# Optimization experiments

Measured on AMD Instinct MI355X. Metric: run time of the kernel, lower is better.

The kernel has to match this reference:

```python
import jax, jax.numpy as jnp
import numpy as np

HEADS = 8


def setup_inputs() -> dict:
    key = jax.random.key(0)
    k1, k2, k3, k4, k5, k6 = jax.random.split(key, 6)
    B, S, E = 2, 2048, 512
    D = E // HEADS
    return {
        "values": jax.random.normal(k1, (B, S, E), dtype=jnp.float32),
        "keys": jax.random.normal(k2, (B, S, E), dtype=jnp.float32),
        "queries": jax.random.normal(k3, (B, S, E), dtype=jnp.float32),
        "mask": jax.random.randint(k4, (B, 1, 1, S), 0, 2, dtype=jnp.int32),
        "W_v": jax.random.normal(k5, (D, D), dtype=jnp.float32) * (1.0 / np.sqrt(D)),
        "W_o": jax.random.normal(k6, (E, E), dtype=jnp.float32) * (1.0 / np.sqrt(E)),
        "b_o": jnp.zeros((E,), dtype=jnp.float32),
    }


def reference(values, keys, queries, mask, W_v, W_o, b_o):
    B, S, E = queries.shape
    H = HEADS
    D = E // H
    # reshape to (b, s, h, d) and apply the SAME W_v linear to v, k, q
    # (faithful to the original, which calls self.values on all three)
    v = jnp.einsum('bshd,ed->bshe', values.reshape(B, -1, H, D), W_v)
    k = jnp.einsum('bshd,ed->bshe', keys.reshape(B, -1, H, D), W_v)
    q = jnp.einsum('bshd,ed->bshe', queries.reshape(B, -1, H, D), W_v)
    # unscaled attention scores (original has no 1/sqrt(d))
    energy = jnp.einsum('bqhd,bkhd->bhqk', q, k)  # (b, h, q, k)
    energy = jnp.where(mask == 0, -jnp.inf, energy)
    attn = jax.nn.softmax(energy, axis=3)
    out = jnp.einsum('bhqk,bkhd->bqhd', attn, v)  # (b, q, h, d)
    out = out.reshape(B, S, E)
    return out @ W_o.T + b_o
```

## Files before the change

kernel.cpp:

```cpp
#include <hip/hip_runtime.h>


#define B_ 2
#define S_ 2048
#define E_ 512
#define H_ 8
#define D_ 64

typedef unsigned short ushort_t;
typedef __attribute__((ext_vector_type(8))) short short8;
typedef __attribute__((ext_vector_type(8))) _Float16 half8;
typedef __attribute__((ext_vector_type(4))) float f32x4;

__device__ __forceinline__ ushort_t f2bs(float x) {
    union { float f; unsigned int u; } a; a.f = x;
    unsigned int u = a.u;
    u += 0x7fffu + ((u >> 16) & 1u);
    return (ushort_t)(u >> 16);
}
__device__ __forceinline__ float bs2f(ushort_t h) {
    union { unsigned int u; float f; } a; a.u = ((unsigned int)h) << 16;
    return a.f;
}
__device__ __forceinline__ ushort_t f2hs(float x) {
    _Float16 h = (_Float16)x;
    ushort_t u; __builtin_memcpy(&u, &h, 2);
    return u;
}
__device__ __forceinline__ void split16(const float4* g, ushort_t* hi, ushort_t* lo) {
    #pragma unroll
    for (int q = 0; q < 4; ++q) {
        float4 f = g[q];
        float vv[4] = {f.x, f.y, f.z, f.w};
        #pragma unroll
        for (int j = 0; j < 4; ++j) {
            ushort_t h = f2bs(vv[j]);
            hi[q * 4 + j] = h;
            lo[q * 4 + j] = f2bs(vv[j] - bs2f(h));
        }
    }
}

__global__ void __launch_bounds__(256) proj_mfma(
    const float* __restrict__ quer, const float* __restrict__ keys,
    const float* __restrict__ vals, const float* __restrict__ Wv,
    ushort_t* __restrict__ qf, ushort_t* __restrict__ kf,
    ushort_t* __restrict__ vt)
{
    __shared__ ushort_t Ah[64 * 72], Al[64 * 72];
    __shared__ ushort_t Bh[64 * 72], Bl[64 * 72];
    const int tens = blockIdx.y;
    const float* src = tens == 0 ? quer : (tens == 1 ? keys : vals);
    const int bx = blockIdx.x;
    const int st = bx & 31, bh = bx >> 5;
    const int b = bh >> 3, h = bh & 7;
    const int s0 = st * 64;
    const int t = threadIdx.x;

    {
        int e = t >> 2, dg = (t & 3) * 16;
        ushort_t th[16], tl[16];
        split16((const float4*)(Wv + e * 64 + dg), th, tl);
        *(uint4*)&Bh[e * 72 + dg] = *(uint4*)th;  *(uint4*)&Bh[e * 72 + dg + 8] = *(uint4*)(th + 8);
        *(uint4*)&Bl[e * 72 + dg] = *(uint4*)tl;  *(uint4*)&Bl[e * 72 + dg + 8] = *(uint4*)(tl + 8);
    }
    {
        int row = t >> 2, cg = (t & 3) * 16;
        const float* g = src + ((size_t)b * S_ + s0 + row) * 512 + h * 64 + cg;
        ushort_t th[16], tl[16];
        split16((const float4*)g, th, tl);
        *(uint4*)&Ah[row * 72 + cg] = *(uint4*)th;  *(uint4*)&Ah[row * 72 + cg + 8] = *(uint4*)(th + 8);
        *(uint4*)&Al[row * 72 + cg] = *(uint4*)tl;  *(uint4*)&Al[row * 72 + cg + 8] = *(uint4*)(tl + 8);
    }
    __syncthreads();

    const int w = t >> 6, lm = t & 15, quad = (t >> 4) & 3;
    f32x4 acc[4];
    #pragma unroll
    for (int nt = 0; nt < 4; ++nt) acc[nt] = (f32x4){0.f, 0.f, 0.f, 0.f};

    #pragma unroll
    for (int kk = 0; kk < 2; ++kk) {
        short8 ah = *(const short8*)&Ah[(w * 16 + lm) * 72 + kk * 32 + quad * 8];
        short8 al = *(const short8*)&Al[(w * 16 + lm) * 72 + kk * 32 + quad * 8];
        #pragma unroll
        for (int nt = 0; nt < 4; ++nt) {
            short8 bh8 = *(const short8*)&Bh[(nt * 16 + lm) * 72 + kk * 32 + quad * 8];
            short8 bl8 = *(const short8*)&Bl[(nt * 16 + lm) * 72 + kk * 32 + quad * 8];
            acc[nt] = __builtin_amdgcn_mfma_f32_16x16x32_bf16(ah, bh8, acc[nt], 0, 0, 0);
            acc[nt] = __builtin_amdgcn_mfma_f32_16x16x32_bf16(al, bh8, acc[nt], 0, 0, 0);
            acc[nt] = __builtin_amdgcn_mfma_f32_16x16x32_bf16(ah, bl8, acc[nt], 0, 0, 0);
        }
    }

    if (tens < 2) {
        ushort_t* dst = tens == 0 ? qf : kf;
        #pragma unroll
        for (int nt = 0; nt < 4; ++nt) {
            #pragma unroll
            for (int r = 0; r < 4; ++r) {
                size_t addr = ((size_t)bh * S_ + s0 + w * 16 + quad * 4 + r) * 64 + nt * 16 + lm;
                dst[addr] = f2hs(acc[nt][r]);
            }
        }
    } else {
        #pragma unroll
        for (int nt = 0; nt < 4; ++nt) {
            unsigned int p0 = (unsigned int)f2bs(acc[nt][0]) | ((unsigned int)f2bs(acc[nt][1]) << 16);
            unsigned int p1 = (unsigned int)f2bs(acc[nt][2]) | ((unsigned int)f2bs(acc[nt][3]) << 16);
            uint2 pk; pk.x = p0; pk.y = p1;
            size_t addr = ((size_t)bh * 64 + nt * 16 + lm) * S_ + s0 + w * 16 + quad * 4;
            *(uint2*)&vt[addr] = pk;
        }
    }
}

__global__ void __launch_bounds__(256) attn_mfma(
    const ushort_t* __restrict__ qf, const ushort_t* __restrict__ kf,
    const ushort_t* __restrict__ vt, const int* __restrict__ mask,
    ushort_t* __restrict__ ctx)
{
    __shared__ ushort_t Ks[64 * 72];
    __shared__ ushort_t Vt[64 * 72];
    __shared__ ushort_t Ps[4 * 16 * 72];
    __shared__ float    mbias[64];

    const int bx = blockIdx.x;
    const int qt = bx & 31;
    const int bh = bx >> 5;
    const int b  = bh >> 3, h = bh & 7;
    const int t  = threadIdx.x;
    const int w = t >> 6, lm = t & 15, quad = (t >> 4) & 3;
    const int q0 = qt * 64;
    const int wbase = w * 16 * 72;

    half8 aq[2];
    {
        size_t qrow = ((size_t)bh * S_ + q0 + w * 16 + lm) * 64 + quad * 8;
        #pragma unroll
        for (int kk = 0; kk < 2; ++kk)
            aq[kk] = *(const half8*)&qf[qrow + kk * 32];
    }
    short8 ones;
    #pragma unroll
    for (int j = 0; j < 8; ++j) ones[j] = (short)0x3F80;

    f32x4 acc[4];
    #pragma unroll
    for (int nt = 0; nt < 4; ++nt) acc[nt] = (f32x4){0.f, 0.f, 0.f, 0.f};
    f32x4 acc_l = (f32x4){0.f, 0.f, 0.f, 0.f};

    for (int kc = 0; kc < S_ / 64; ++kc) {
        __syncthreads();
        {
            int row = t >> 2, cg = (t & 3) * 16;
            size_t gaddr = ((size_t)bh * S_ + kc * 64 + row) * 64 + cg;
            *(uint4*)&Ks[row * 72 + cg]     = *(const uint4*)&kf[gaddr];
            *(uint4*)&Ks[row * 72 + cg + 8] = *(const uint4*)&kf[gaddr + 8];
        }
        {
            int row = t >> 2, cg = (t & 3) * 16;
            size_t gaddr = ((size_t)bh * 64 + row) * S_ + kc * 64 + cg;
            *(uint4*)&Vt[row * 72 + cg]     = *(const uint4*)&vt[gaddr];
            *(uint4*)&Vt[row * 72 + cg + 8] = *(const uint4*)&vt[gaddr + 8];
        }
        if (t < 64) mbias[t] = mask[b * S_ + kc * 64 + t] ? -64.f : -1e30f;
        __syncthreads();

        #pragma unroll
        for (int nt = 0; nt < 4; ++nt) {
            f32x4 s = (f32x4){0.f, 0.f, 0.f, 0.f};
            #pragma unroll
            for (int kk = 0; kk < 2; ++kk) {
                half8 bk = *(const half8*)&Ks[(nt * 16 + lm) * 72 + kk * 32 + quad * 8];
                s = __builtin_amdgcn_mfma_f32_16x16x32_f16(aq[kk], bk, s, 0, 0, 0);
            }
            float mv = mbias[nt * 16 + lm];
            #pragma unroll
            for (int r = 0; r < 4; ++r) {
                float p = __expf(s[r] + mv);
                Ps[wbase + (quad * 4 + r) * 72 + nt * 16 + lm] = f2bs(p);
            }
        }
        __builtin_amdgcn_s_waitcnt(0);

        #pragma unroll
        for (int kk = 0; kk < 2; ++kk) {
            short8 ap = *(const short8*)&Ps[wbase + lm * 72 + kk * 32 + quad * 8];
            #pragma unroll
            for (int nt = 0; nt < 4; ++nt) {
                short8 bv = *(const short8*)&Vt[(nt * 16 + lm) * 72 + kk * 32 + quad * 8];
                acc[nt] = __builtin_amdgcn_mfma_f32_16x16x32_bf16(ap, bv, acc[nt], 0, 0, 0);
            }
            acc_l = __builtin_amdgcn_mfma_f32_16x16x32_bf16(ap, ones, acc_l, 0, 0, 0);
        }
    }

    #pragma unroll
    for (int r = 0; r < 4; ++r) {
        float inv = 1.f / acc_l[r];
        int s = q0 + w * 16 + quad * 4 + r;
        #pragma unroll
        for (int nt = 0; nt < 4; ++nt) {
            int d = nt * 16 + lm;
            ctx[((size_t)b * S_ + s) * E_ + h * D_ + d] = f2bs(acc[nt][r] * inv);
        }
    }
}

__global__ void __launch_bounds__(256) outproj_mfma(
    const ushort_t* __restrict__ ctx, const float* __restrict__ Wo,
    const float* __restrict__ bo, float* __restrict__ out)
{
    __shared__ ushort_t As[64 * 72];
    __shared__ ushort_t Bs[64 * 72];
    const int m0 = blockIdx.x * 64, n0 = blockIdx.y * 64;
    const int t = threadIdx.x;
    const int w = t >> 6, lm = t & 15, quad = (t >> 4) & 3;

    f32x4 acc[4];
    #pragma unroll
    for (int nt = 0; nt < 4; ++nt) acc[nt] = (f32x4){0.f, 0.f, 0.f, 0.f};

    for (int kc = 0; kc < E_ / 64; ++kc) {
        __syncthreads();
        {
            int row = t >> 2, cg = (t & 3) * 16;
            const ushort_t* g = ctx + (size_t)(m0 + row) * E_ + kc * 64 + cg;
            *(uint4*)&As[row * 72 + cg]     = *(const uint4*)g;
            *(uint4*)&As[row * 72 + cg + 8] = *(const uint4*)(g + 8);
        }
        {
            int n = t >> 2, kg = (t & 3) * 16;
            const float4* g = (const float4*)(Wo + (size_t)(n0 + n) * E_ + kc * 64 + kg);
            ushort_t tmp[16];
            #pragma unroll
            for (int q = 0; q < 4; ++q) {
                float4 f = g[q];
                tmp[q * 4 + 0] = f2bs(f.x); tmp[q * 4 + 1] = f2bs(f.y);
                tmp[q * 4 + 2] = f2bs(f.z); tmp[q * 4 + 3] = f2bs(f.w);
            }
            *(uint4*)&Bs[n * 72 + kg]     = *(uint4*)tmp;
            *(uint4*)&Bs[n * 72 + kg + 8] = *(uint4*)(tmp + 8);
        }
        __syncthreads();

        #pragma unroll
        for (int kk = 0; kk < 2; ++kk) {
            short8 a = *(const short8*)&As[(w * 16 + lm) * 72 + kk * 32 + quad * 8];
            #pragma unroll
            for (int nt = 0; nt < 4; ++nt) {
                short8 bb = *(const short8*)&Bs[(nt * 16 + lm) * 72 + kk * 32 + quad * 8];
                acc[nt] = __builtin_amdgcn_mfma_f32_16x16x32_bf16(a, bb, acc[nt], 0, 0, 0);
            }
        }
    }

    #pragma unroll
    for (int nt = 0; nt < 4; ++nt) {
        float bias = bo[n0 + nt * 16 + lm];
        #pragma unroll
        for (int r = 0; r < 4; ++r) {
            int m = m0 + w * 16 + quad * 4 + r;
            out[(size_t)m * E_ + n0 + nt * 16 + lm] = acc[nt][r] + bias;
        }
    }
}

extern "C" void kernel_launch(void* const* d_in, const int* in_sizes, int n_in,
                              void* d_out, int out_size, void* d_ws, size_t ws_size,
                              hipStream_t stream) {
    const float* vals = (const float*)d_in[0];
    const float* keys = (const float*)d_in[1];
    const float* quer = (const float*)d_in[2];
    const int*   mask = (const int*)d_in[3];
    const float* Wv   = (const float*)d_in[4];
    const float* Wo   = (const float*)d_in[5];
    const float* bo   = (const float*)d_in[6];
    float* out = (float*)d_out;

    const size_t N = (size_t)B_ * H_ * S_ * D_;
    ushort_t* ws  = (ushort_t*)d_ws;
    ushort_t* qf  = ws;
    ushort_t* kf  = ws + N;
    ushort_t* vt  = ws + 2 * N;
    ushort_t* ctx = ws + 3 * N;

    proj_mfma<<<dim3(B_ * H_ * (S_ / 64), 3), 256, 0, stream>>>(
        quer, keys, vals, Wv, qf, kf, vt);
    attn_mfma<<<B_ * H_ * (S_ / 64), 256, 0, stream>>>(qf, kf, vt, mask, ctx);
    outproj_mfma<<<dim3((B_ * S_) / 64, E_ / 64), 256, 0, stream>>>(ctx, Wo, bo, out);
}
```

Baseline: 147.8 us.

## Double-buffer K/V tiles in attention with register prefetch and transposed score MFMA

Attention K/V and mask tiles are now double-buffered in shared memory. The next tile is loaded into registers while the current tile is computed, then written to the alternate buffer, which cuts the loop to one barrier per iteration and hides global load latency. The score MFMA operands are also swapped, so each lane holds four consecutive keys and can read the mask bias as a vector and store P with one packed 8-byte write instead of four scalar stores. The cost is twice the LDS for K/V, more live registers, and a narrower waitcnt (lgkmcnt only).

```diff
diff --git a/kernel.cpp b/kernel.cpp
--- a/kernel.cpp
+++ b/kernel.cpp
@@ -120,26 +120,29 @@
     const ushort_t* __restrict__ vt, const int* __restrict__ mask,
     ushort_t* __restrict__ ctx)
 {
-    __shared__ ushort_t Ks[64 * 72];
-    __shared__ ushort_t Vt[64 * 72];
+    __shared__ ushort_t Ks[2][64 * 72];
+    __shared__ ushort_t Vt[2][64 * 72];
     __shared__ ushort_t Ps[4 * 16 * 72];
-    __shared__ float    mbias[64];
+    __shared__ float    mb[2][64];
 
     const int bx = blockIdx.x;
     const int qt = bx & 31;
     const int bh = bx >> 5;
-    const int b  = bh >> 3, h = bh & 7;
+    const int b  = bh >> 3;
     const int t  = threadIdx.x;
     const int w = t >> 6, lm = t & 15, quad = (t >> 4) & 3;
     const int q0 = qt * 64;
     const int wbase = w * 16 * 72;
 
+    const int srow = t >> 2, scg = (t & 3) * 16;
+    const size_t kgbase = ((size_t)bh * S_ + srow) * 64 + scg;
+    const size_t vgbase = ((size_t)bh * 64 + srow) * S_ + scg;
+
     half8 aq[2];
     {
         size_t qrow = ((size_t)bh * S_ + q0 + w * 16 + lm) * 64 + quad * 8;
-        #pragma unroll
-        for (int kk = 0; kk < 2; ++kk)
-            aq[kk] = *(const half8*)&qf[qrow + kk * 32];
+        aq[0] = *(const half8*)&qf[qrow];
+        aq[1] = *(const half8*)&qf[qrow + 32];
     }
     short8 ones;
     #pragma unroll
@@ -150,52 +153,77 @@
     for (int nt = 0; nt < 4; ++nt) acc[nt] = (f32x4){0.f, 0.f, 0.f, 0.f};
     f32x4 acc_l = (f32x4){0.f, 0.f, 0.f, 0.f};
 
+    {
+        *(uint4*)&Ks[0][srow * 72 + scg]     = *(const uint4*)&kf[kgbase];
+        *(uint4*)&Ks[0][srow * 72 + scg + 8] = *(const uint4*)&kf[kgbase + 8];
+        *(uint4*)&Vt[0][srow * 72 + scg]     = *(const uint4*)&vt[vgbase];
+        *(uint4*)&Vt[0][srow * 72 + scg + 8] = *(const uint4*)&vt[vgbase + 8];
+        if (t < 64) mb[0][t] = mask[b * S_ + t] ? -64.f : -1e30f;
+    }
+    __syncthreads();
+
+    int cur = 0;
     for (int kc = 0; kc < S_ / 64; ++kc) {
-        __syncthreads();
-        {
-            int row = t >> 2, cg = (t & 3) * 16;
-            size_t gaddr = ((size_t)bh * S_ + kc * 64 + row) * 64 + cg;
-            *(uint4*)&Ks[row * 72 + cg]     = *(const uint4*)&kf[gaddr];
-            *(uint4*)&Ks[row * 72 + cg + 8] = *(const uint4*)&kf[gaddr + 8];
-        }
-        {
-            int row = t >> 2, cg = (t & 3) * 16;
-            size_t gaddr = ((size_t)bh * 64 + row) * S_ + kc * 64 + cg;
-            *(uint4*)&Vt[row * 72 + cg]     = *(const uint4*)&vt[gaddr];
-            *(uint4*)&Vt[row * 72 + cg + 8] = *(const uint4*)&vt[gaddr + 8];
-        }
-        if (t < 64) mbias[t] = mask[b * S_ + kc * 64 + t] ? -64.f : -1e30f;
-        __syncthreads();
+        const bool pf = (kc + 1) < (S_ / 64);
+
+        uint4 pk0, pk1, pv0, pv1; int mnext = 0;
+        if (pf) {
+            size_t ka = kgbase + (size_t)(kc + 1) * 64 * 64;
+            pk0 = *(const uint4*)&kf[ka];
+            pk1 = *(const uint4*)&kf[ka + 8];
+            size_t va = vgbase + (size_t)(kc + 1) * 64;
+            pv0 = *(const uint4*)&vt[va];
+            pv1 = *(const uint4*)&vt[va + 8];
+            if (t < 64) mnext = mask[b * S_ + (kc + 1) * 64 + t];
+        }
+
+        const ushort_t* Kc = Ks[cur];
+        const ushort_t* Vc = Vt[cur];
 
         #pragma unroll
         for (int nt = 0; nt < 4; ++nt) {
             f32x4 s = (f32x4){0.f, 0.f, 0.f, 0.f};
             #pragma unroll
             for (int kk = 0; kk < 2; ++kk) {
-                half8 bk = *(const half8*)&Ks[(nt * 16 + lm) * 72 + kk * 32 + quad * 8];
-                s = __builtin_amdgcn_mfma_f32_16x16x32_f16(aq[kk], bk, s, 0, 0, 0);
-            }
-            float mv = mbias[nt * 16 + lm];
-            #pragma unroll
-            for (int r = 0; r < 4; ++r) {
-                float p = __expf(s[r] + mv);
-                Ps[wbase + (quad * 4 + r) * 72 + nt * 16 + lm] = f2bs(p);
-            }
-        }
-        __builtin_amdgcn_s_waitcnt(0);
+                half8 ak = *(const half8*)&Kc[(nt * 16 + lm) * 72 + kk * 32 + quad * 8];
+                s = __builtin_amdgcn_mfma_f32_16x16x32_f16(ak, aq[kk], s, 0, 0, 0);
+            }
+            f32x4 mv = *(const f32x4*)&mb[cur][nt * 16 + quad * 4];
+            float p0 = __expf(s[0] + mv[0]);
+            float p1 = __expf(s[1] + mv[1]);
+            float p2 = __expf(s[2] + mv[2]);
+            float p3 = __expf(s[3] + mv[3]);
+            uint2 pkd;
+            pkd.x = (unsigned int)f2bs(p0) | ((unsigned int)f2bs(p1) << 16);
+            pkd.y = (unsigned int)f2bs(p2) | ((unsigned int)f2bs(p3) << 16);
+            *(uint2*)&Ps[wbase + lm * 72 + nt * 16 + quad * 4] = pkd;
+        }
+        asm volatile("s_waitcnt lgkmcnt(0)" ::: "memory");
 
         #pragma unroll
         for (int kk = 0; kk < 2; ++kk) {
             short8 ap = *(const short8*)&Ps[wbase + lm * 72 + kk * 32 + quad * 8];
             #pragma unroll
             for (int nt = 0; nt < 4; ++nt) {
-                short8 bv = *(const short8*)&Vt[(nt * 16 + lm) * 72 + kk * 32 + quad * 8];
+                short8 bv = *(const short8*)&Vc[(nt * 16 + lm) * 72 + kk * 32 + quad * 8];
                 acc[nt] = __builtin_amdgcn_mfma_f32_16x16x32_bf16(ap, bv, acc[nt], 0, 0, 0);
             }
             acc_l = __builtin_amdgcn_mfma_f32_16x16x32_bf16(ap, ones, acc_l, 0, 0, 0);
         }
-    }
-
+
+        if (pf) {
+            const int nxt = cur ^ 1;
+            *(uint4*)&Ks[nxt][srow * 72 + scg]     = pk0;
+            *(uint4*)&Ks[nxt][srow * 72 + scg + 8] = pk1;
+            *(uint4*)&Vt[nxt][srow * 72 + scg]     = pv0;
+            *(uint4*)&Vt[nxt][srow * 72 + scg + 8] = pv1;
+            if (t < 64) mb[nxt][t] = mnext ? -64.f : -1e30f;
+            __syncthreads();
+        }
+        cur ^= 1;
+    }
+
+    const int h = bh & 7;
     #pragma unroll
     for (int r = 0; r < 4; ++r) {
         float inv = 1.f / acc_l[r];
```

Result: faster. 140.1 us (-5.2%).
